# Kernel optimization log

Hardware: AMD Instinct MI355X
Metric: run time of the kernel (lower is better)

## Reference

```python
import jax, jax.numpy as jnp
from jax import lax
import numpy as np

T, B, I, H, O = 1000, 256, 128, 512, 32
ALPHA = 20.0 / 100.0  # dt / tau
EXC_RATIO = 0.8
SPARSITY = 0.2


def setup_inputs() -> dict:
    key = jax.random.key(0)
    ks = jax.random.split(key, 8)
    x = jax.random.normal(ks[0], (T, B, I), dtype=jnp.float32)
    w_in = jax.random.normal(ks[1], (H, I), dtype=jnp.float32) * (1.0 / np.sqrt(I))
    b_in = jax.random.uniform(ks[2], (H,), dtype=jnp.float32, minval=-1, maxval=1) / np.sqrt(I)
    w_h = jax.random.normal(ks[3], (H, H), dtype=jnp.float32) * (1.0 / np.sqrt(H))
    b_h = jax.random.uniform(ks[4], (H,), dtype=jnp.float32, minval=-1, maxval=1) / np.sqrt(H)
    n_exc = int(H * EXC_RATIO)
    dale = jnp.where(jnp.arange(H) < n_exc, 1.0, -1.0).astype(jnp.float32)
    # sparse mask: rand < sparsity, diagonal forced True
    sp = (jax.random.uniform(ks[5], (H, H)) < SPARSITY).astype(jnp.float32)
    sparse = jnp.maximum(sp, jnp.eye(H, dtype=jnp.float32))
    fc_w = jax.random.normal(ks[6], (O, H), dtype=jnp.float32) * (1.0 / np.sqrt(H))
    fc_b = jax.random.uniform(ks[7], (O,), dtype=jnp.float32, minval=-1, maxval=1) / np.sqrt(H)
    return {"x": x, "w_in": w_in, "b_in": b_in, "w_h": w_h, "b_h": b_h,
            "dale": dale, "sparse": sparse, "fc_w": fc_w, "fc_b": fc_b}


def reference(x, w_in, b_in, w_h, b_h, dale, sparse, fc_w, fc_b):
    alpha = jnp.float32(ALPHA)
    oma = jnp.float32(1.0 - ALPHA)
    # effective recurrent weight: relu(W) * dale (per presynaptic column) * sparse mask
    w_eff = jax.nn.relu(w_h) * dale[None, :] * sparse  # [H, H]
    # precompute input drive for all timesteps: [T, B, H]
    x_drive = jnp.einsum('tbi,hi->tbh', x, w_in) + b_in

    def step(carry, xd_t):
        state, out = carry
        total = xd_t + out @ w_eff.T + b_h  # [B, H]
        state = state * oma + total * alpha
        out = jax.nn.relu(state)
        return (state, out), out

    init = (jnp.zeros((B, H), x.dtype), jnp.zeros((B, H), x.dtype))
    _, rnn_activity = lax.scan(step, init, x_drive)  # [T, B, H]
    out = jnp.einsum('tbh,oh->tbo', rnn_activity, fc_w) + fc_b  # [T, B, O]
    return out, rnn_activity
```

## Files before the change

### kernel.cpp

```cpp
#include <hip/hip_runtime.h>

#define T_STEPS 1000
#define BATCH   256
#define IN_DIM  128
#define HID     512
#define OUT_DIM 32
#define ALPHA_F 0.2f
#define OMA_F   0.8f
#define MAXNNZ  96
#define BDEPTH  20


__global__ __launch_bounds__(512) void build_rank_kernel(
    const float* __restrict__ w_h, const float* __restrict__ sparse,
    unsigned int* __restrict__ perm, unsigned int* __restrict__ nnzR)
{
    int tid = threadIdx.x;
    __shared__ int cnt_sh[HID];

    const float4* wr4 = (const float4*)(w_h    + tid * HID);
    const float4* sr4 = (const float4*)(sparse + tid * HID);
    int cnt = 0;
    for (int j4 = 0; j4 < HID / 4; j4++) {
        float4 w = wr4[j4];
        float4 s = sr4[j4];
        if (w.x > 0.f && s.x > 0.5f) cnt++;
        if (w.y > 0.f && s.y > 0.5f) cnt++;
        if (w.z > 0.f && s.z > 0.5f) cnt++;
        if (w.w > 0.f && s.w > 0.5f) cnt++;
    }
    int c = min(cnt, MAXNNZ);

    cnt_sh[tid] = c;
    __syncthreads();
    int rank = 0;
    for (int j = 0; j < HID; j++) {
        int cj = cnt_sh[j];
        rank += (cj < c) || (cj == c && j < tid);
    }
    perm[rank] = (unsigned int)tid;
    nnzR[rank] = (unsigned int)c;
}

__global__ __launch_bounds__(64) void fill_kernel(
    const float* __restrict__ w_h, const float* __restrict__ dale,
    const float* __restrict__ sparse,
    const unsigned int* __restrict__ perm, const unsigned int* __restrict__ nnzR,
    float* __restrict__ val_t, unsigned short* __restrict__ idx_t)
{
    int r    = blockIdx.x;
    int lane = threadIdx.x;
    int h = (int)perm[r];
    int c = (int)nnzR[r];

    float*          vout = val_t + r * MAXNNZ;
    unsigned short* iout = idx_t + r * MAXNNZ;

    for (int k = lane; k < MAXNNZ; k += 64)
        if (k >= c) { vout[k] = 0.f; iout[k] = 0; }

    unsigned long long lt = (1ull << lane) - 1ull;
    int pos_base = 0;
#pragma unroll
    for (int ch = 0; ch < 8; ch++) {
        int j = ch * 64 + lane;
        float w = w_h[h * HID + j];
        float s = sparse[h * HID + j];
        bool pred = (w > 0.f) && (s > 0.5f);
        unsigned long long m = __ballot(pred);
        if (pred) {
            int pos = pos_base + (int)__popcll(m & lt);
            if (pos < MAXNNZ) {
                vout[pos] = w * dale[j];
                iout[pos] = (unsigned short)(j * 4);
            }
        }
        pos_base += (int)__popcll(m);
    }
}

__global__ __launch_bounds__(64) void sched_kernel(
    float* __restrict__ val_t, unsigned short* __restrict__ idx_t,
    unsigned int* __restrict__ nnzR)
{
    int w    = blockIdx.x;
    int lane = threadIdx.x;
    int rank = w * 64 + lane;
    int g    = lane >> 5;
    int l32  = lane & 31;

    __shared__ unsigned short entb[64][32][BDEPTH];
    __shared__ unsigned char  cntb[64][32];
    __shared__ unsigned char  outsrc[64][MAXNNZ];
    __shared__ float          vll[64][MAXNNZ];
    __shared__ volatile int   wbuf[2][32];

    int c = (int)nnzR[rank];
    int S = c;
#pragma unroll
    for (int off = 32; off; off >>= 1) S = max(S, __shfl_xor(S, off));

    for (int b = 0; b < 32; b++) cntb[lane][b] = 0;
    for (int e = 0; e < MAXNNZ; e++) {
        vll[lane][e]    = val_t[rank * MAXNNZ + e];
        outsrc[lane][e] = 255;
    }
    unsigned int bm = 0;
    int rem = 0;
    for (int e = 0; e < c; e++) {
        int word = ((int)idx_t[rank * MAXNNZ + e]) >> 2;
        int b = word & 31;
        int k = (int)cntb[lane][b];
        if (k < BDEPTH) {
            entb[lane][b][k] = (unsigned short)((e << 9) | word);
            cntb[lane][b] = (unsigned char)(k + 1);
            bm |= 1u << b;
            rem++;
        }
    }

    for (int s = 0; s < MAXNNZ; s++) {
        if (s < S) {
            unsigned int claimed = 0;
            int myb = -1;
#pragma unroll
            for (int round = 0; round < 2; round++) {
                int prop = -1;
                if (myb < 0 && rem > 0) {
                    unsigned int avail = bm & ~claimed;
                    if (avail) {
                        int rot = (l32 * 7 + s * 3 + round * 11) & 31;
                        unsigned int av2 = (avail >> rot) | (avail << ((32 - rot) & 31));
                        prop = (__ffs(av2) - 1 + rot) & 31;
                    }
                }
                if (prop >= 0) wbuf[g][prop] = lane;
                int won = 0;
                if (prop >= 0 && wbuf[g][prop] == lane) { myb = prop; won = 1; }
                unsigned int cm = won ? (1u << myb) : 0u;
#pragma unroll
                for (int off = 16; off; off >>= 1)
                    cm |= (unsigned int)__shfl_xor((int)cm, off, 32);
                claimed |= cm;
            }
            if (myb < 0 && rem > 0 && rem >= S - s) {
                unsigned int a = bm & ~claimed;
                myb = a ? (__ffs(a) - 1) : (__ffs(bm) - 1);
            }
            if (myb >= 0) {
                int k = (int)cntb[lane][myb] - 1;
                unsigned short pk = entb[lane][myb][k];
                cntb[lane][myb] = (unsigned char)k;
                if (k == 0) bm &= ~(1u << myb);
                outsrc[lane][s] = (unsigned char)(pk >> 9);
                idx_t[rank * MAXNNZ + s] = (unsigned short)((pk & 511) * 4);
                rem--;
            } else {
                unsigned int freeb = ~claimed;
                int pb = freeb ? (__ffs(freeb) - 1) : 0;
                idx_t[rank * MAXNNZ + s] = (unsigned short)(pb * 4);
            }
        } else {
            idx_t[rank * MAXNNZ + s] = 0;
        }
    }
    nnzR[rank] = (unsigned int)S;

    for (int s = 0; s < MAXNNZ; s++) {
        int src = outsrc[lane][s];
        val_t[rank * MAXNNZ + s] = (src == 255) ? 0.f : vll[lane][src];
    }
}

__global__ __launch_bounds__(256) void trans_kernel(
    const float* __restrict__ w_in, const float* __restrict__ fc_w,
    float* __restrict__ w_inT, float* __restrict__ fcT)
{
    int o = blockIdx.x * 256 + threadIdx.x;
    if (o < IN_DIM * HID) {
        int k = o / HID, n = o % HID;
        w_inT[o] = w_in[n * IN_DIM + k];
    } else {
        int o2 = o - IN_DIM * HID;
        if (o2 < HID * OUT_DIM) {
            int k = o2 / OUT_DIM, oo = o2 % OUT_DIM;
            fcT[o2] = fc_w[oo * HID + k];
        }
    }
}

__global__ __launch_bounds__(256, 4) void ingemm_kernel(
    const float* __restrict__ x, const float* __restrict__ w_inT,
    const float* __restrict__ b_in, const float* __restrict__ b_h,
    float* __restrict__ xd)
{
    __shared__ float xl[256 * 33];
    int tid = threadIdx.x;
    int B  = blockIdx.x;
    int r8 = B & 7;
    int tt = B >> 3;
    int nc = tt & 15;
    int aa = tt >> 4;
    int mb = 8 * aa + r8;
    long m0 = (long)mb * 256;
    int n0 = nc * 32;

    float acc[32];
#pragma unroll
    for (int j = 0; j < 32; j++) acc[j] = b_in[n0 + j] + b_h[n0 + j];

    for (int k0 = 0; k0 < IN_DIM; k0 += 32) {
        __syncthreads();
#pragma unroll
        for (int i = 0; i < 8; i++) {
            int f  = tid + i * 256;
            int rr = f >> 3, cc = f & 7;
            float4 v = *(const float4*)(x + (m0 + rr) * IN_DIM + k0 + cc * 4);
            float* d = &xl[rr * 33 + cc * 4];
            d[0] = v.x; d[1] = v.y; d[2] = v.z; d[3] = v.w;
        }
        __syncthreads();
        const float* xrow = &xl[tid * 33];
#pragma unroll
        for (int kk = 0; kk < 32; kk++) {
            float a = xrow[kk];
            const float* wrow = w_inT + (k0 + kk) * HID + n0;
#pragma unroll
            for (int j = 0; j < 32; j++) acc[j] = fmaf(a, wrow[j], acc[j]);
        }
    }
    float* orow = xd + (m0 + tid) * HID + n0;
#pragma unroll
    for (int j = 0; j < 8; j++)
        *(float4*)(orow + j * 4) =
            make_float4(acc[4*j], acc[4*j+1], acc[4*j+2], acc[4*j+3]);
}


#define PAIR2(base, ii)                                              \
    {                                                                \
        unsigned int pk = idp[ii];                                   \
        float g0 = *(const float*)((base) + (pk & 0xffffu));         \
        float g1 = *(const float*)((base) + (pk >> 16));             \
        a0 = fmaf(val[2*(ii)],     g0, a0);                          \
        a1 = fmaf(val[2*(ii) + 1], g1, a1);                          \
    }

#define CHUNK2(base, c)                                              \
    PAIR2(base, 2*(c)+0) PAIR2(base, 2*(c)+1)

__device__ __forceinline__ float sparse_accum(
    const char* base, const float (&val)[MAXNNZ],
    const unsigned int (&idp)[MAXNNZ / 2], int nch, float a_init)
{
    float a0 = a_init, a1 = 0.f;
    switch (nch) {
        case 24: CHUNK2(base, 23) [[fallthrough]];
        case 23: CHUNK2(base, 22) [[fallthrough]];
        case 22: CHUNK2(base, 21) [[fallthrough]];
        case 21: CHUNK2(base, 20) [[fallthrough]];
        case 20: CHUNK2(base, 19) [[fallthrough]];
        case 19: CHUNK2(base, 18) [[fallthrough]];
        case 18: CHUNK2(base, 17) [[fallthrough]];
        case 17: CHUNK2(base, 16) [[fallthrough]];
        case 16: CHUNK2(base, 15) [[fallthrough]];
        case 15: CHUNK2(base, 14) [[fallthrough]];
        case 14: CHUNK2(base, 13) [[fallthrough]];
        case 13: CHUNK2(base, 12) [[fallthrough]];
        case 12: CHUNK2(base, 11) [[fallthrough]];
        case 11: CHUNK2(base, 10) [[fallthrough]];
        case 10: CHUNK2(base,  9) [[fallthrough]];
        case  9: CHUNK2(base,  8) [[fallthrough]];
        case  8: CHUNK2(base,  7) [[fallthrough]];
        case  7: CHUNK2(base,  6) [[fallthrough]];
        case  6: CHUNK2(base,  5) [[fallthrough]];
        case  5: CHUNK2(base,  4) [[fallthrough]];
        case  4: CHUNK2(base,  3) [[fallthrough]];
        case  3: CHUNK2(base,  2) [[fallthrough]];
        case  2: CHUNK2(base,  1) [[fallthrough]];
        case  1: CHUNK2(base,  0) break;
        default: break;
    }
    return a0 + a1;
}

__global__ __launch_bounds__(512, 2) void scan_kernel(
    float* __restrict__ act_g,
    const float* __restrict__ val_t, const unsigned short* __restrict__ idx_t,
    const unsigned int* __restrict__ perm, const unsigned int* __restrict__ nnzR)
{
    int tid = threadIdx.x;
    int b   = blockIdx.x;
    __shared__ float sbuf[1024];
    sbuf[tid] = 0.f;

    float        val[MAXNNZ];
    unsigned int idp[MAXNNZ / 2];
    {
        const float4* vp = (const float4*)(val_t + tid * MAXNNZ);
#pragma unroll
        for (int i = 0; i < MAXNNZ / 4; i++) {
            float4 v = vp[i];
            val[4*i] = v.x; val[4*i+1] = v.y; val[4*i+2] = v.z; val[4*i+3] = v.w;
        }
        const uint4* ip = (const uint4*)(idx_t + tid * MAXNNZ);
#pragma unroll
        for (int i = 0; i < MAXNNZ / 8; i++) {
            uint4 u = ip[i];
            idp[4*i] = u.x; idp[4*i+1] = u.y; idp[4*i+2] = u.z; idp[4*i+3] = u.w;
        }
    }
    int h = (int)perm[tid];
    int wmax = (int)nnzR[tid | 63];
    wmax = __builtin_amdgcn_readfirstlane(wmax);
    int nch = (wmax + 3) >> 2;

    float state = 0.f;
    int gi = b * HID + h;
    float xdv = act_g[gi];
    const char* sb = (const char*)sbuf;
    __syncthreads();

    for (int t = 0; t < T_STEPS; t += 2) {
        {
            float xn = act_g[gi + BATCH * HID];
            float a = sparse_accum(sb, val, idp, nch, xdv);
            state = state * OMA_F + a * ALPHA_F;
            float act = fmaxf(state, 0.f);
            sbuf[512 + h] = act;
            __syncthreads();
            act_g[gi] = act;
            gi += BATCH * HID;
            xdv = xn;
        }
        {
            int gn = (t < T_STEPS - 2) ? gi + BATCH * HID : gi;
            float xn = act_g[gn];
            float a = sparse_accum(sb + 2048, val, idp, nch, xdv);
            state = state * OMA_F + a * ALPHA_F;
            float act = fmaxf(state, 0.f);
            sbuf[h] = act;
            __syncthreads();
            act_g[gi] = act;
            gi += BATCH * HID;
            xdv = xn;
        }
    }
}

__global__ __launch_bounds__(256, 4) void outgemm_kernel(
    const float* __restrict__ act_g, const float* __restrict__ fcT,
    const float* __restrict__ fc_b, float* __restrict__ out_g)
{
    __shared__ float al[256 * 33];
    int tid = threadIdx.x;
    long m0 = (long)blockIdx.x * 256;

    float acc[32];
#pragma unroll
    for (int o = 0; o < 32; o++) acc[o] = fc_b[o];

    for (int k0 = 0; k0 < HID; k0 += 32) {
        __syncthreads();
#pragma unroll
        for (int i = 0; i < 8; i++) {
            int f  = tid + i * 256;
            int rr = f >> 3, cc = f & 7;
            float4 v = *(const float4*)(act_g + (m0 + rr) * HID + k0 + cc * 4);
            float* d = &al[rr * 33 + cc * 4];
            d[0] = v.x; d[1] = v.y; d[2] = v.z; d[3] = v.w;
        }
        __syncthreads();
        const float* arow = &al[tid * 33];
#pragma unroll
        for (int kk = 0; kk < 32; kk++) {
            float a = arow[kk];
            const float* frow = fcT + (k0 + kk) * OUT_DIM;
#pragma unroll
            for (int o = 0; o < 32; o++) acc[o] = fmaf(a, frow[o], acc[o]);
        }
    }
    float* orow = out_g + (m0 + tid) * OUT_DIM;
#pragma unroll
    for (int j = 0; j < 8; j++)
        *(float4*)(orow + j * 4) =
            make_float4(acc[4*j], acc[4*j+1], acc[4*j+2], acc[4*j+3]);
}

extern "C" void kernel_launch(void* const* d_in, const int* in_sizes, int n_in,
                              void* d_out, int out_size, void* d_ws, size_t ws_size,
                              hipStream_t stream)
{
    const float* x      = (const float*)d_in[0];
    const float* w_in   = (const float*)d_in[1];
    const float* b_in   = (const float*)d_in[2];
    const float* w_h    = (const float*)d_in[3];
    const float* b_h    = (const float*)d_in[4];
    const float* dale   = (const float*)d_in[5];
    const float* sparse = (const float*)d_in[6];
    const float* fc_w   = (const float*)d_in[7];
    const float* fc_b   = (const float*)d_in[8];

    float* out_g = (float*)d_out;
    float* act_g = out_g + (long)T_STEPS * BATCH * OUT_DIM;

    char* ws = (char*)d_ws;
    float*          val_t = (float*)(ws + 0);
    unsigned short* idx_t = (unsigned short*)(ws + 196608);
    unsigned int*   perm  = (unsigned int*)(ws + 294912);
    unsigned int*   nnzR  = (unsigned int*)(ws + 296960);
    float*          w_inT = (float*)(ws + 299008);
    float*          fcT   = (float*)(ws + 561152);

    build_rank_kernel<<<1, 512, 0, stream>>>(w_h, sparse, perm, nnzR);
    fill_kernel<<<HID, 64, 0, stream>>>(w_h, dale, sparse, perm, nnzR, val_t, idx_t);
    sched_kernel<<<8, 64, 0, stream>>>(val_t, idx_t, nnzR);
    trans_kernel<<<320, 256, 0, stream>>>(w_in, fc_w, w_inT, fcT);
    ingemm_kernel<<<16000, 256, 0, stream>>>(x, w_inT, b_in, b_h, act_g);
    scan_kernel<<<256, 512, 0, stream>>>(act_g, val_t, idx_t, perm, nnzR);
    outgemm_kernel<<<1000, 256, 0, stream>>>(act_g, fcT, fc_b, out_g);
}
```

Before: 2.010 ms.

## Fuse input GEMM, recurrent scan and output GEMM into one per-batch kernel

Merges the three kernels into a single kernel with one block per batch element. Each block first computes the input drive for its batch row across all timesteps, then runs the recurrent scan, then applies the output projection, with block barriers and fences between phases. This removes two launches and the inter-kernel gaps. In exchange the two GEMMs run on only 256 blocks instead of thousands, so they use far less of the GPU's parallelism and may become slower phases.

```diff
diff --git a/kernel.cpp b/kernel.cpp
--- a/kernel.cpp
+++ b/kernel.cpp
@@ -187,53 +187,6 @@
             fcT[o2] = fc_w[oo * HID + k];
         }
     }
-}
-
-__global__ __launch_bounds__(256, 4) void ingemm_kernel(
-    const float* __restrict__ x, const float* __restrict__ w_inT,
-    const float* __restrict__ b_in, const float* __restrict__ b_h,
-    float* __restrict__ xd)
-{
-    __shared__ float xl[256 * 33];
-    int tid = threadIdx.x;
-    int B  = blockIdx.x;
-    int r8 = B & 7;
-    int tt = B >> 3;
-    int nc = tt & 15;
-    int aa = tt >> 4;
-    int mb = 8 * aa + r8;
-    long m0 = (long)mb * 256;
-    int n0 = nc * 32;
-
-    float acc[32];
-#pragma unroll
-    for (int j = 0; j < 32; j++) acc[j] = b_in[n0 + j] + b_h[n0 + j];
-
-    for (int k0 = 0; k0 < IN_DIM; k0 += 32) {
-        __syncthreads();
-#pragma unroll
-        for (int i = 0; i < 8; i++) {
-            int f  = tid + i * 256;
-            int rr = f >> 3, cc = f & 7;
-            float4 v = *(const float4*)(x + (m0 + rr) * IN_DIM + k0 + cc * 4);
-            float* d = &xl[rr * 33 + cc * 4];
-            d[0] = v.x; d[1] = v.y; d[2] = v.z; d[3] = v.w;
-        }
-        __syncthreads();
-        const float* xrow = &xl[tid * 33];
-#pragma unroll
-        for (int kk = 0; kk < 32; kk++) {
-            float a = xrow[kk];
-            const float* wrow = w_inT + (k0 + kk) * HID + n0;
-#pragma unroll
-            for (int j = 0; j < 32; j++) acc[j] = fmaf(a, wrow[j], acc[j]);
-        }
-    }
-    float* orow = xd + (m0 + tid) * HID + n0;
-#pragma unroll
-    for (int j = 0; j < 8; j++)
-        *(float4*)(orow + j * 4) =
-            make_float4(acc[4*j], acc[4*j+1], acc[4*j+2], acc[4*j+3]);
 }
 
 
@@ -284,107 +237,169 @@
     return a0 + a1;
 }
 
-__global__ __launch_bounds__(512, 2) void scan_kernel(
+__global__ __launch_bounds__(512, 2) void fused_kernel(
+    const float* __restrict__ x, const float* __restrict__ w_inT,
+    const float* __restrict__ b_in, const float* __restrict__ b_h,
     float* __restrict__ act_g,
     const float* __restrict__ val_t, const unsigned short* __restrict__ idx_t,
-    const unsigned int* __restrict__ perm, const unsigned int* __restrict__ nnzR)
-{
+    const unsigned int* __restrict__ perm, const unsigned int* __restrict__ nnzR,
+    const float* __restrict__ fcT, const float* __restrict__ fc_b,
+    float* __restrict__ out_g)
+{
+    __shared__ float smem[1024 + 512 * 33];
     int tid = threadIdx.x;
     int b   = blockIdx.x;
-    __shared__ float sbuf[1024];
-    sbuf[tid] = 0.f;
-
-    float        val[MAXNNZ];
-    unsigned int idp[MAXNNZ / 2];
+
     {
-        const float4* vp = (const float4*)(val_t + tid * MAXNNZ);
-#pragma unroll
-        for (int i = 0; i < MAXNNZ / 4; i++) {
-            float4 v = vp[i];
-            val[4*i] = v.x; val[4*i+1] = v.y; val[4*i+2] = v.z; val[4*i+3] = v.w;
-        }
-        const uint4* ip = (const uint4*)(idx_t + tid * MAXNNZ);
-#pragma unroll
-        for (int i = 0; i < MAXNNZ / 8; i++) {
-            uint4 u = ip[i];
-            idp[4*i] = u.x; idp[4*i+1] = u.y; idp[4*i+2] = u.z; idp[4*i+3] = u.w;
-        }
-    }
-    int h = (int)perm[tid];
-    int wmax = (int)nnzR[tid | 63];
-    wmax = __builtin_amdgcn_readfirstlane(wmax);
-    int nch = (wmax + 3) >> 2;
-
-    float state = 0.f;
-    int gi = b * HID + h;
-    float xdv = act_g[gi];
-    const char* sb = (const char*)sbuf;
+        float* xl = smem + 1024;
+        int r = tid & 63;
+        int g = tid >> 6;
+        for (int mt = 0; mt < 16; mt++) {
+            int t0 = mt * 64;
+            for (int nc = 0; nc < 2; nc++) {
+                int n0 = nc * 256 + g * 32;
+                float acc[32];
+#pragma unroll
+                for (int j = 0; j < 32; j++) acc[j] = b_in[n0 + j] + b_h[n0 + j];
+                for (int k0 = 0; k0 < IN_DIM; k0 += 32) {
+                    __syncthreads();
+                    {
+                        int rr = tid >> 3, cc = tid & 7;
+                        if (t0 + rr < T_STEPS) {
+                            float4 v = *(const float4*)(
+                                x + ((t0 + rr) * BATCH + b) * IN_DIM + k0 + cc * 4);
+                            float* d = &xl[rr * 33 + cc * 4];
+                            d[0] = v.x; d[1] = v.y; d[2] = v.z; d[3] = v.w;
+                        }
+                    }
+                    __syncthreads();
+                    if (t0 + r < T_STEPS) {
+                        const float* xrow = &xl[r * 33];
+#pragma unroll
+                        for (int kk = 0; kk < 32; kk++) {
+                            float a = xrow[kk];
+                            const float* wrow = w_inT + (k0 + kk) * HID + n0;
+#pragma unroll
+                            for (int j = 0; j < 32; j++)
+                                acc[j] = fmaf(a, wrow[j], acc[j]);
+                        }
+                    }
+                }
+                if (t0 + r < T_STEPS) {
+                    float* orow = act_g + ((t0 + r) * BATCH + b) * HID + n0;
+#pragma unroll
+                    for (int j = 0; j < 8; j++)
+                        *(float4*)(orow + j * 4) =
+                            make_float4(acc[4*j], acc[4*j+1], acc[4*j+2], acc[4*j+3]);
+                }
+            }
+        }
+    }
     __syncthreads();
-
-    for (int t = 0; t < T_STEPS; t += 2) {
+    __threadfence();
+
+    {
+        float* sbuf = smem;
+        sbuf[tid] = 0.f;
+
+        float        val[MAXNNZ];
+        unsigned int idp[MAXNNZ / 2];
         {
-            float xn = act_g[gi + BATCH * HID];
-            float a = sparse_accum(sb, val, idp, nch, xdv);
-            state = state * OMA_F + a * ALPHA_F;
-            float act = fmaxf(state, 0.f);
-            sbuf[512 + h] = act;
-            __syncthreads();
-            act_g[gi] = act;
-            gi += BATCH * HID;
-            xdv = xn;
-        }
-        {
-            int gn = (t < T_STEPS - 2) ? gi + BATCH * HID : gi;
-            float xn = act_g[gn];
-            float a = sparse_accum(sb + 2048, val, idp, nch, xdv);
-            state = state * OMA_F + a * ALPHA_F;
-            float act = fmaxf(state, 0.f);
-            sbuf[h] = act;
-            __syncthreads();
-            act_g[gi] = act;
-            gi += BATCH * HID;
-            xdv = xn;
-        }
-    }
-}
-
-__global__ __launch_bounds__(256, 4) void outgemm_kernel(
-    const float* __restrict__ act_g, const float* __restrict__ fcT,
-    const float* __restrict__ fc_b, float* __restrict__ out_g)
-{
-    __shared__ float al[256 * 33];
-    int tid = threadIdx.x;
-    long m0 = (long)blockIdx.x * 256;
-
-    float acc[32];
-#pragma unroll
-    for (int o = 0; o < 32; o++) acc[o] = fc_b[o];
-
-    for (int k0 = 0; k0 < HID; k0 += 32) {
+            const float4* vp = (const float4*)(val_t + tid * MAXNNZ);
+#pragma unroll
+            for (int i = 0; i < MAXNNZ / 4; i++) {
+                float4 v = vp[i];
+                val[4*i] = v.x; val[4*i+1] = v.y; val[4*i+2] = v.z; val[4*i+3] = v.w;
+            }
+            const uint4* ip = (const uint4*)(idx_t + tid * MAXNNZ);
+#pragma unroll
+            for (int i = 0; i < MAXNNZ / 8; i++) {
+                uint4 u = ip[i];
+                idp[4*i] = u.x; idp[4*i+1] = u.y; idp[4*i+2] = u.z; idp[4*i+3] = u.w;
+            }
+        }
+        int h = (int)perm[tid];
+        int wmax = (int)nnzR[tid | 63];
+        wmax = __builtin_amdgcn_readfirstlane(wmax);
+        int nch = (wmax + 3) >> 2;
+
+        float state = 0.f;
+        int gi = b * HID + h;
+        float xdv = act_g[gi];
+        const char* sb = (const char*)sbuf;
         __syncthreads();
-#pragma unroll
-        for (int i = 0; i < 8; i++) {
-            int f  = tid + i * 256;
-            int rr = f >> 3, cc = f & 7;
-            float4 v = *(const float4*)(act_g + (m0 + rr) * HID + k0 + cc * 4);
-            float* d = &al[rr * 33 + cc * 4];
-            d[0] = v.x; d[1] = v.y; d[2] = v.z; d[3] = v.w;
-        }
-        __syncthreads();
-        const float* arow = &al[tid * 33];
-#pragma unroll
-        for (int kk = 0; kk < 32; kk++) {
-            float a = arow[kk];
-            const float* frow = fcT + (k0 + kk) * OUT_DIM;
-#pragma unroll
-            for (int o = 0; o < 32; o++) acc[o] = fmaf(a, frow[o], acc[o]);
-        }
-    }
-    float* orow = out_g + (m0 + tid) * OUT_DIM;
-#pragma unroll
-    for (int j = 0; j < 8; j++)
-        *(float4*)(orow + j * 4) =
-            make_float4(acc[4*j], acc[4*j+1], acc[4*j+2], acc[4*j+3]);
+
+        for (int t = 0; t < T_STEPS; t += 2) {
+            {
+                float xn = act_g[gi + BATCH * HID];
+                float a = sparse_accum(sb, val, idp, nch, xdv);
+                state = state * OMA_F + a * ALPHA_F;
+                float act = fmaxf(state, 0.f);
+                sbuf[512 + h] = act;
+                __syncthreads();
+                act_g[gi] = act;
+                gi += BATCH * HID;
+                xdv = xn;
+            }
+            {
+                int gn = (t < T_STEPS - 2) ? gi + BATCH * HID : gi;
+                float xn = act_g[gn];
+                float a = sparse_accum(sb + 2048, val, idp, nch, xdv);
+                state = state * OMA_F + a * ALPHA_F;
+                float act = fmaxf(state, 0.f);
+                sbuf[h] = act;
+                __syncthreads();
+                act_g[gi] = act;
+                gi += BATCH * HID;
+                xdv = xn;
+            }
+        }
+    }
+    __syncthreads();
+    __threadfence();
+
+    {
+        float* al = smem + 1024;
+        for (int mt2 = 0; mt2 < 2; mt2++) {
+            int t0 = mt2 * 512;
+            int t  = t0 + tid;
+            float acc[32];
+#pragma unroll
+            for (int o = 0; o < 32; o++) acc[o] = fc_b[o];
+            for (int k0 = 0; k0 < HID; k0 += 32) {
+                __syncthreads();
+#pragma unroll
+                for (int i = 0; i < 8; i++) {
+                    int f = tid + i * 512, rr = f >> 3, cc = f & 7;
+                    if (t0 + rr < T_STEPS) {
+                        float4 v = *(const float4*)(
+                            act_g + ((t0 + rr) * BATCH + b) * HID + k0 + cc * 4);
+                        float* d = &al[rr * 33 + cc * 4];
+                        d[0] = v.x; d[1] = v.y; d[2] = v.z; d[3] = v.w;
+                    }
+                }
+                __syncthreads();
+                if (t < T_STEPS) {
+                    const float* arow = &al[tid * 33];
+#pragma unroll
+                    for (int kk = 0; kk < 32; kk++) {
+                        float a = arow[kk];
+                        const float* frow = fcT + (k0 + kk) * OUT_DIM;
+#pragma unroll
+                        for (int o = 0; o < 32; o++)
+                            acc[o] = fmaf(a, frow[o], acc[o]);
+                    }
+                }
+            }
+            if (t < T_STEPS) {
+                float* orow = out_g + (t * BATCH + b) * OUT_DIM;
+#pragma unroll
+                for (int j = 0; j < 8; j++)
+                    *(float4*)(orow + j * 4) =
+                        make_float4(acc[4*j], acc[4*j+1], acc[4*j+2], acc[4*j+3]);
+            }
+        }
+    }
 }
 
 extern "C" void kernel_launch(void* const* d_in, const int* in_sizes, int n_in,
@@ -416,7 +431,7 @@
     fill_kernel<<<HID, 64, 0, stream>>>(w_h, dale, sparse, perm, nnzR, val_t, idx_t);
     sched_kernel<<<8, 64, 0, stream>>>(val_t, idx_t, nnzR);
     trans_kernel<<<320, 256, 0, stream>>>(w_in, fc_w, w_inT, fcT);
-    ingemm_kernel<<<16000, 256, 0, stream>>>(x, w_inT, b_in, b_h, act_g);
-    scan_kernel<<<256, 512, 0, stream>>>(act_g, val_t, idx_t, perm, nnzR);
-    outgemm_kernel<<<1000, 256, 0, stream>>>(act_g, fcT, fc_b, out_g);
-}
+    fused_kernel<<<BATCH, 512, 0, stream>>>(x, w_inT, b_in, b_h, act_g,
+                                            val_t, idx_t, perm, nnzR,
+                                            fcT, fc_b, out_g);
+}
```

Measured after the change: 3.911 ms. 94.6% more time.

## Split each hidden unit's sparse dot product across two half-blocks of threads

Applied to the files above, without the earlier changes.

The scan kernel now launches 1024 threads per batch element. Each hidden row's nonzero list is split into two halves, and the two halves are handled by two threads. The second thread writes its partial sum to shared memory, and the first thread combines the two partials and updates the state. This halves the per-thread serial gather chain and the register footprint on the latency-bound recurrence. The cost is an extra __syncthreads per timestep and only one block per CU.

```diff
diff --git a/kernel.cpp b/kernel.cpp
--- a/kernel.cpp
+++ b/kernel.cpp
@@ -9,6 +9,7 @@
 #define OMA_F   0.8f
 #define MAXNNZ  96
 #define BDEPTH  20
+#define HSLOT   48
 
 
 __global__ __launch_bounds__(512) void build_rank_kernel(
@@ -250,23 +251,11 @@
     PAIR2(base, 2*(c)+0) PAIR2(base, 2*(c)+1)
 
 __device__ __forceinline__ float sparse_accum(
-    const char* base, const float (&val)[MAXNNZ],
-    const unsigned int (&idp)[MAXNNZ / 2], int nch, float a_init)
+    const char* base, const float (&val)[HSLOT],
+    const unsigned int (&idp)[HSLOT / 2], int nch, float a_init)
 {
     float a0 = a_init, a1 = 0.f;
     switch (nch) {
-        case 24: CHUNK2(base, 23) [[fallthrough]];
-        case 23: CHUNK2(base, 22) [[fallthrough]];
-        case 22: CHUNK2(base, 21) [[fallthrough]];
-        case 21: CHUNK2(base, 20) [[fallthrough]];
-        case 20: CHUNK2(base, 19) [[fallthrough]];
-        case 19: CHUNK2(base, 18) [[fallthrough]];
-        case 18: CHUNK2(base, 17) [[fallthrough]];
-        case 17: CHUNK2(base, 16) [[fallthrough]];
-        case 16: CHUNK2(base, 15) [[fallthrough]];
-        case 15: CHUNK2(base, 14) [[fallthrough]];
-        case 14: CHUNK2(base, 13) [[fallthrough]];
-        case 13: CHUNK2(base, 12) [[fallthrough]];
         case 12: CHUNK2(base, 11) [[fallthrough]];
         case 11: CHUNK2(base, 10) [[fallthrough]];
         case 10: CHUNK2(base,  9) [[fallthrough]];
@@ -284,64 +273,88 @@
     return a0 + a1;
 }
 
-__global__ __launch_bounds__(512, 2) void scan_kernel(
+__global__ __launch_bounds__(1024) void scan_kernel(
     float* __restrict__ act_g,
     const float* __restrict__ val_t, const unsigned short* __restrict__ idx_t,
     const unsigned int* __restrict__ perm, const unsigned int* __restrict__ nnzR)
 {
     int tid = threadIdx.x;
+    int r   = tid & 511;
+    int isB = tid >> 9;
     int b   = blockIdx.x;
     __shared__ float sbuf[1024];
-    sbuf[tid] = 0.f;
-
-    float        val[MAXNNZ];
-    unsigned int idp[MAXNNZ / 2];
+    __shared__ float pbuf[512];
+    sbuf[tid & 1023] = 0.f;
+
+    int S = (int)nnzR[r | 63];
+    S = __builtin_amdgcn_readfirstlane(S);
+    int nchT = (S + 3) >> 2;
+    int nchA = (nchT + 1) >> 1;
+    int nch  = isB ? (nchT - nchA) : nchA;
+    int base = isB ? (nchA << 2) : 0;
+
+    float        val[HSLOT];
+    unsigned int idp[HSLOT / 2];
     {
-        const float4* vp = (const float4*)(val_t + tid * MAXNNZ);
-#pragma unroll
-        for (int i = 0; i < MAXNNZ / 4; i++) {
+        const float4* vp = (const float4*)(val_t + r * MAXNNZ + base);
+#pragma unroll
+        for (int i = 0; i < HSLOT / 4; i++) {
             float4 v = vp[i];
             val[4*i] = v.x; val[4*i+1] = v.y; val[4*i+2] = v.z; val[4*i+3] = v.w;
         }
-        const uint4* ip = (const uint4*)(idx_t + tid * MAXNNZ);
-#pragma unroll
-        for (int i = 0; i < MAXNNZ / 8; i++) {
-            uint4 u = ip[i];
-            idp[4*i] = u.x; idp[4*i+1] = u.y; idp[4*i+2] = u.z; idp[4*i+3] = u.w;
-        }
-    }
-    int h = (int)perm[tid];
-    int wmax = (int)nnzR[tid | 63];
-    wmax = __builtin_amdgcn_readfirstlane(wmax);
-    int nch = (wmax + 3) >> 2;
+        const uint2* ip = (const uint2*)(idx_t + r * MAXNNZ + base);
+#pragma unroll
+        for (int i = 0; i < HSLOT / 4; i++) {
+            uint2 u = ip[i];
+            idp[2*i] = u.x; idp[2*i+1] = u.y;
+        }
+    }
+    int h = (int)perm[r];
 
     float state = 0.f;
     int gi = b * HID + h;
-    float xdv = act_g[gi];
+    float xdv = 0.f;
+    if (!isB) xdv = act_g[gi];
     const char* sb = (const char*)sbuf;
     __syncthreads();
 
     for (int t = 0; t < T_STEPS; t += 2) {
         {
-            float xn = act_g[gi + BATCH * HID];
-            float a = sparse_accum(sb, val, idp, nch, xdv);
-            state = state * OMA_F + a * ALPHA_F;
-            float act = fmaxf(state, 0.f);
-            sbuf[512 + h] = act;
+            float xn = 0.f;
+            if (!isB) xn = act_g[gi + BATCH * HID];
+            float ap = sparse_accum(sb, val, idp, nch, isB ? 0.f : xdv);
+            if (isB) pbuf[r] = ap;
             __syncthreads();
-            act_g[gi] = act;
+            float act = 0.f;
+            if (!isB) {
+                float a = ap + pbuf[r];
+                state = state * OMA_F + a * ALPHA_F;
+                act = fmaxf(state, 0.f);
+                sbuf[512 + h] = act;
+            }
+            __syncthreads();
+            if (!isB) act_g[gi] = act;
             gi += BATCH * HID;
             xdv = xn;
         }
         {
-            int gn = (t < T_STEPS - 2) ? gi + BATCH * HID : gi;
-            float xn = act_g[gn];
-            float a = sparse_accum(sb + 2048, val, idp, nch, xdv);
-            state = state * OMA_F + a * ALPHA_F;
-            float act = fmaxf(state, 0.f);
-            sbuf[h] = act;
+            float xn = 0.f;
+            if (!isB) {
+                int gn = (t < T_STEPS - 2) ? gi + BATCH * HID : gi;
+                xn = act_g[gn];
+            }
+            float ap = sparse_accum(sb + 2048, val, idp, nch, isB ? 0.f : xdv);
+            if (isB) pbuf[r] = ap;
             __syncthreads();
-            act_g[gi] = act;
+            float act = 0.f;
+            if (!isB) {
+                float a = ap + pbuf[r];
+                state = state * OMA_F + a * ALPHA_F;
+                act = fmaxf(state, 0.f);
+                sbuf[h] = act;
+            }
+            __syncthreads();
+            if (!isB) act_g[gi] = act;
             gi += BATCH * HID;
             xdv = xn;
         }
@@ -417,6 +430,6 @@
     sched_kernel<<<8, 64, 0, stream>>>(val_t, idx_t, nnzR);
     trans_kernel<<<320, 256, 0, stream>>>(w_in, fc_w, w_inT, fcT);
     ingemm_kernel<<<16000, 256, 0, stream>>>(x, w_inT, b_in, b_h, act_g);
-    scan_kernel<<<256, 512, 0, stream>>>(act_g, val_t, idx_t, perm, nnzR);
+    scan_kernel<<<256, 1024, 0, stream>>>(act_g, val_t, idx_t, perm, nnzR);
     outgemm_kernel<<<1000, 256, 0, stream>>>(act_g, fcT, fc_b, out_g);
 }
```

Result: slower. 2.063 ms (+2.6%).
